# Kernel tuning notes

Measured on AMD Instinct MI355X. Metric: run time of the kernel, lower is better.

Reference implementation:

```python
import math
import jax, jax.numpy as jnp
import numpy as np

RM = 100.0      # r_max
RN = 1000       # r_dsc
LMAX = 2
MATCH_FRAC = 0.1
PARA1 = 1.0
RD = RM / RN    # radial step
NE = 4096       # batch of trial energies


def setup_inputs() -> dict:
    key = jax.random.key(0)
    # small negative energies (bound-state regime) to keep the exponential
    # Numerov growth over 900 steps within fp32 range
    init_energy = -(jax.random.uniform(key, (NE,), dtype=jnp.float32) * 0.01 + 0.005)
    return {"init_energy": init_energy}


def _disc_solve(sol0, factor, limit):
    # sol0: (5, n_e, L) initial 5-point window; factor: (rn, n_e, L)
    # Numerov-style 4-step recurrence, vectorized coefficients + lax.scan
    c = 3.0 / 40.0 * RD ** 2
    idx = jnp.arange(1, limit - 5)
    f0 = factor[idx]
    f1 = factor[idx + 1]
    f2 = factor[idx + 2]
    f3 = factor[idx + 3]
    f4 = factor[idx + 4]
    denom = 1.0 - c * f4
    a = -1.0 + c * f0 / denom
    b = 2.0 + (13.0 / 15.0) * RD ** 2 * f1 / denom
    cc = -2.0 + (7.0 / 60.0) * RD ** 2 * f2 / denom
    d = 2.0 + (13.0 / 15.0) * RD ** 2 * f3 / denom

    def step(prev, coef):
        ca, cb, ccc, cd = coef
        new4 = ca * prev[1] + cb * prev[2] + ccc * prev[3] + cd * prev[4]
        new = jnp.concatenate([prev[1:], new4[None]], axis=0)  # shift window
        return new, new

    _, rest = jax.lax.scan(step, sol0, (a, b, cc, d))
    return jnp.concatenate([sol0[None], rest], axis=0)  # (limit-5, 5, n_e, L)


def _derivative(func, at):
    return (25.0 * func[at - 1] - 48.0 * func[at - 2] + 36.0 * func[at - 3]
            - 16.0 * func[at - 4] + 3.0 * func[at - 5]) / (12.0 * RD)


def _integrate(func):
    # faithful to original: integrand squares `func` again (func is u**2 here)
    M = func.shape[0] // 4 - 1
    g0 = func[0:4 * M:4]
    g1 = func[1:4 * M:4]
    g2 = func[2:4 * M:4]
    g3 = func[3:4 * M:4]
    g4 = func[4::4][:M]
    integrand = (7.0 * (g0 ** 2 + g4 ** 2) + 32.0 * (g1 ** 2 + g3 ** 2)
                 + 12.0 * g2) * (2.0 * RD / 45.0)
    return integrand.sum(axis=0)


def _forward(init_energy):
    L = LMAX + 1
    dt = init_energy.dtype
    n_e = init_energy.shape[0]
    r = jnp.linspace(RM / RN, RM, RN, dtype=dt).reshape(RN, 1, 1)
    l = jnp.arange(L, dtype=dt).reshape(1, 1, L)

    energy = jnp.broadcast_to(init_energy[:, None], (n_e, L))  # (n_e, L)
    e_val = energy[None]                                       # (1, n_e, L)
    # coulomb potential -1/r; factor: (rn, n_e, L)
    factor = l * (l + 1) / r ** 2 + PARA1 * (-e_val - 1.0 / r)

    # left (r->0) initial window: u ~ r^(l+1) + r^(l+2)/(2(l+1)) * (-para_1)
    r0 = jnp.linspace(RD, 5 * RD, 5, dtype=dt).reshape(5, 1, 1)
    u_zero_init = jnp.broadcast_to(
        r0 ** (l + 1) - r0 ** (l + 2) / (2.0 * (l + 1)) * PARA1, (5, n_e, L))

    # right (r->r_max) initial window: r * truncated spherical-bessel series
    r_inf = jnp.linspace(RM - 4 * RD, RM, 5, dtype=dt).reshape(5, 1, 1)
    fact = jnp.array([math.prod([2 * li + 1 for li in range(lm + 1)])
                      for lm in range(L)], dtype=dt)  # [1, 3, 15]
    x = r_inf * jnp.sqrt(jnp.abs(e_val))              # (5, n_e, L)
    base = x ** l / fact
    t1 = x ** 2 / 2.0 / (2 * l + 3)
    t2 = (x ** 2 / 2.0) ** 2 / (2.0 * (2 * l + 3) * (2 * l + 5))
    u_infty_init = jnp.broadcast_to(r_inf * (base * (1.0 + t1 + t2)), (5, n_e, L))

    match = int(RN * MATCH_FRAC)  # 100
    uz = _disc_solve(u_zero_init, factor, match)                     # (95, 5, n_e, L)
    ui = _disc_solve(u_infty_init, factor[::-1], RN - match)[::-1]   # (895, 5, n_e, L)
    u_zero = jnp.concatenate([uz[0], uz[:, 4]], axis=0)    # (100, n_e, L)
    u_infty = jnp.concatenate([ui[0], ui[:, 4]], axis=0)   # (900, n_e, L)

    lfunc_in = _derivative(u_zero, match) / u_zero[-1]
    # faithful: the trailing flip acts on the energy axis of the (n_e, L) result
    lfunc_out = _derivative(u_infty[::-1], RN - match)[::-1] / u_infty[0]
    integ_in = _integrate(u_zero ** 2)
    integ_out = _integrate(u_infty ** 2)
    delta = -(lfunc_out - lfunc_in) / (integ_in / u_zero[-1] ** 2
                                       + integ_out / u_infty[0] ** 2)
    return (energy + delta, u_zero, u_infty)


def reference(init_energy):
    return _forward(init_energy)
```

## Files before the change

kernel.cpp:

```cpp
#include <hip/hip_runtime.h>


namespace {
constexpr int kNE    = 4096;
constexpr int kNCH   = kNE * 3;
constexpr int kMatch = 100;
constexpr float kC   = 3.0f / 40.0f * 0.01f;
constexpr float kK1  = 13.0f / 15.0f * 0.01f;
constexpr float kK2  = 7.0f / 60.0f * 0.01f;
constexpr int kSeg        = 32;
constexpr int kCPB        = 16;
constexpr int kZeroBlocks = kNCH / 512;
constexpr int kInfBlocks  = kNCH / kCPB;
}

__device__ __forceinline__ float rcp_f(float x) { return __builtin_amdgcn_rcpf(x); }
__device__ __forceinline__ float rcp_nr(float x) {
    float r = __builtin_amdgcn_rcpf(x);
    return fmaf(fmaf(-x, r, 1.0f), r, r);
}

__global__ __launch_bounds__(512) void solve_kernel(const float* __restrict__ energy,
                                                    float* __restrict__ out,
                                                    float* __restrict__ ws)
{
    __shared__ float gt[899 * 3];
    __shared__ float sPT[16][kSeg - 1][kCPB];
    __shared__ float sSt[kSeg][kCPB][4];
    float* sR4 = &sPT[0][0][0];
    float* sR2 = sR4 + kSeg * kCPB;

    const int bid = (int)blockIdx.x;
    const int tid = (int)threadIdx.x;
    float* uzero = out + kNCH;
    float* uinf  = out + kNCH + (size_t)kMatch * kNCH;

    if (bid < kZeroBlocks) {
        const int t  = bid * 512 + tid;
        const int l  = t % 3;
        const int ei = t / 3;
        const float e = energy[ei], negE = -e;
        const float ll1 = (float)(l * (l + 1));
        const float rdiv = (l == 0) ? 0.5f : ((l == 1) ? 0.25f : (1.0f/6.0f));
        float p0,p1,p2,p3,p4;
        {
            float pw[5];
            #pragma unroll
            for (int k = 0; k < 5; ++k) {
                float r = 0.1f * (float)(k + 1);
                float rl1 = (l == 0) ? r : ((l == 1) ? r*r : r*r*r);
                pw[k] = rl1 - (rl1 * r) * rdiv;
                uzero[(size_t)k * kNCH + t] = pw[k];
            }
            uzero[(size_t)5 * kNCH + t] = pw[4];
            p0=pw[0]; p1=pw[1]; p2=pw[2]; p3=pw[3]; p4=pw[4];
        }
        float acc4, acc2;
        {
            float q0=p0*p0, q1=p1*p1, q2=p2*p2, q3=p3*p3, q4=p4*p4;
            acc4 = 7.0f*q0*q0 + 32.0f*q1*q1 + 32.0f*q3*q3 + 14.0f*q4*q4 + 32.0f*q4*q4;
            acc2 = q2;
        }
        float f0, f1, f2, f3;
        {
            float i1 = rcp_f(0.2f), i2 = rcp_f(0.3f), i3 = rcp_f(0.4f), i4 = rcp_f(0.5f);
            f0 = fmaf(i1, fmaf(ll1, i1, -1.0f), negE);
            f1 = fmaf(i2, fmaf(ll1, i2, -1.0f), negE);
            f2 = fmaf(i3, fmaf(ll1, i3, -1.0f), negE);
            f3 = fmaf(i4, fmaf(ll1, i4, -1.0f), negE);
        }
        float* ptr = uzero + (size_t)6 * kNCH + t;
        #pragma unroll 4
        for (int j = 5; j <= 98; ++j) {
            float ri = rcp_f(fmaf((float)j, 0.1f, 0.1f));
            float f4 = fmaf(ri, fmaf(ll1, ri, -1.0f), negE);
            float iv = rcp_f(fmaf(-kC, f4, 1.0f));
            float a  = fmaf(kC  * f0, iv, -1.0f);
            float b  = fmaf(kK1 * f1, iv,  2.0f);
            float cc = fmaf(kK2 * f2, iv, -2.0f);
            float d  = fmaf(kK1 * f3, iv,  2.0f);
            float nw = fmaf(d, p4, fmaf(cc, p3, fmaf(b, p2, a * p1)));
            *ptr = nw; ptr += kNCH;
            float v2 = nw*nw, v4 = v2*v2;
            if (j <= 94) {
                int m = (j + 1) & 3;
                if (m == 2)      acc2 += v2;
                else if (m == 0) acc4 += 14.0f * v4;
                else             acc4 += 32.0f * v4;
            } else if (j == 95) {
                acc4 += 7.0f * v4;
            }
            f0 = f1; f1 = f2; f2 = f3; f3 = f4;
            p0 = p1; p1 = p2; p2 = p3; p3 = p4; p4 = nw;
        }
        float integ = fmaf(12.0f, acc2, acc4) * (2.0f * 0.1f / 45.0f);
        float deriv = fmaf(25.0f, p4, fmaf(-48.0f, p3, fmaf(36.0f, p2,
                      fmaf(-16.0f, p1, 3.0f * p0)))) * (1.0f / 1.2f);
        ws[2 * kNCH + t] = deriv / p4;
        ws[3 * kNCH + t] = integ / (p4 * p4);
        return;
    }

    for (int j = tid; j < 899; j += 512) {
        float ri = rcp_nr(fmaf((float)j, -0.1f, 100.0f));
        gt[j * 3 + 0] = -ri;
        gt[j * 3 + 1] = ri * fmaf(2.0f, ri, -1.0f);
        gt[j * 3 + 2] = ri * fmaf(6.0f, ri, -1.0f);
    }
    __syncthreads();

    const int b = bid - kZeroBlocks;
    const int g = tid & 15;
    const int s = tid >> 4;
    const int t = b * kCPB + g;
    const int l  = t % 3;
    const int ei = t / 3;
    const float e = energy[ei], negE = -e;
    const int jstart = 5 + 28 * s;

    const float ff0 = gt[(jstart - 4) * 3 + l] + negE;
    const float ff1 = gt[(jstart - 3) * 3 + l] + negE;
    const float ff2 = gt[(jstart - 2) * 3 + l] + negE;
    const float ff3 = gt[(jstart - 1) * 3 + l] + negE;
    float F0 = ff0, F1 = ff1, F2 = ff2, F3 = ff3;
    const float* gp0 = &gt[jstart * 3 + l];
    const float* gp = gp0;

    float ca, cb, cc_, cd;
#define COEF(FA,FB,FC,FD) \
    { float f4 = *gp + negE; gp += 3; \
      float x  = kC * f4; \
      float iv = fmaf(x, x, x) + 1.0f; \
      ca  = fmaf(kC  * FA, iv, -1.0f); \
      cb  = fmaf(kK1 * FB, iv,  2.0f); \
      cc_ = fmaf(kK2 * FC, iv, -2.0f); \
      cd  = fmaf(kK1 * FD, iv,  2.0f); \
      FA = f4; }

#define MSTEP(FA,FB,FC,FD,RA,RB,RC,RD) \
    { COEF(FA,FB,FC,FD) \
      RA[0] = fmaf(cd,RD[0], fmaf(cc_,RC[0], fmaf(cb,RB[0], ca*RA[0]))); \
      RA[1] = fmaf(cd,RD[1], fmaf(cc_,RC[1], fmaf(cb,RB[1], ca*RA[1]))); \
      RA[2] = fmaf(cd,RD[2], fmaf(cc_,RC[2], fmaf(cb,RB[2], ca*RA[2]))); \
      RA[3] = fmaf(cd,RD[3], fmaf(cc_,RC[3], fmaf(cb,RB[3], ca*RA[3]))); }

    if (s < kSeg - 1) {
        float ra[4] = {1,0,0,0}, rb[4] = {0,1,0,0}, rc[4] = {0,0,1,0}, rd[4] = {0,0,0,1};
        for (int it = 0; it < 7; ++it) {
            MSTEP(F0,F1,F2,F3, ra,rb,rc,rd)
            MSTEP(F1,F2,F3,F0, rb,rc,rd,ra)
            MSTEP(F2,F3,F0,F1, rc,rd,ra,rb)
            MSTEP(F3,F0,F1,F2, rd,ra,rb,rc)
        }
        #pragma unroll
        for (int c = 0; c < 4; ++c) {
            sPT[0*4+c][s][g] = ra[c];
            sPT[1*4+c][s][g] = rb[c];
            sPT[2*4+c][s][g] = rc[c];
            sPT[3*4+c][s][g] = rd[c];
        }
    }
    __syncthreads();

    if (s == 0) {
        const float se  = sqrtf(fabsf(e));
        const float rfc = (l == 0) ? 1.0f : ((l == 1) ? (1.0f/3.0f) : (1.0f/15.0f));
        const float rt1 = (l == 0) ? (1.0f/3.0f) : ((l == 1) ? (1.0f/5.0f) : (1.0f/7.0f));
        const float rt2 = (l == 0) ? (1.0f/30.0f) : ((l == 1) ? (1.0f/70.0f) : (1.0f/126.0f));
        float pw[5];
        #pragma unroll
        for (int k = 0; k < 5; ++k) {
            float rinf = 99.6f + 0.1f * (float)k;
            float x  = rinf * se;
            float xl = (l == 0) ? 1.0f : ((l == 1) ? x : x * x);
            float h  = x * x * 0.5f;
            pw[k] = rinf * (xl * rfc * (1.0f + h * rt1 + (h * h) * rt2));
        }
        uinf[(size_t)899 * kNCH + t] = pw[4];
        float st0 = pw[1], st1 = pw[2], st2 = pw[3], st3 = pw[4];
        for (int ss = 0; ss < kSeg; ++ss) {
            sSt[ss][g][0] = st0; sSt[ss][g][1] = st1;
            sSt[ss][g][2] = st2; sSt[ss][g][3] = st3;
            if (ss < kSeg - 1) {
                float n0 = fmaf(sPT[ 3][ss][g],st3, fmaf(sPT[ 2][ss][g],st2,
                           fmaf(sPT[ 1][ss][g],st1, sPT[ 0][ss][g]*st0)));
                float n1 = fmaf(sPT[ 7][ss][g],st3, fmaf(sPT[ 6][ss][g],st2,
                           fmaf(sPT[ 5][ss][g],st1, sPT[ 4][ss][g]*st0)));
                float n2 = fmaf(sPT[11][ss][g],st3, fmaf(sPT[10][ss][g],st2,
                           fmaf(sPT[ 9][ss][g],st1, sPT[ 8][ss][g]*st0)));
                float n3 = fmaf(sPT[15][ss][g],st3, fmaf(sPT[14][ss][g],st2,
                           fmaf(sPT[13][ss][g],st1, sPT[12][ss][g]*st0)));
                st0 = n0; st1 = n1; st2 = n2; st3 = n3;
            }
        }
    }
    __syncthreads();

    gp = gp0;
    F0 = ff0; F1 = ff1; F2 = ff2; F3 = ff3;
    int j = jstart;
    float p0 = sSt[s][g][0], p1 = sSt[s][g][1], p2 = sSt[s][g][2], p3 = sSt[s][g][3];
    float acc4 = 0.0f, acc2 = 0.0f;
    float* ptr = uinf + (size_t)(903 - jstart) * kNCH + t;
#define RSTEP(FA,FB,FC,FD,PA,PB,PC,PD) \
    { COEF(FA,FB,FC,FD) \
      float nw = fmaf(cd,PD, fmaf(cc_,PC, fmaf(cb,PB, ca*PA))); \
      PA = nw; *ptr = nw; ptr -= kNCH; \
      float v2 = nw*nw, v4 = v2*v2; \
      if (j >= 8) { int m = j & 3; \
        if (m == 1) acc2 += v2; \
        else acc4 += ((m == 3) ? 14.0f : 32.0f) * v4; } \
      else if (j == 7) acc4 += 7.0f * v4; \
      ++j; }

    float h0 = 0.0f;
    if (s < kSeg - 1) {
        for (int it = 0; it < 7; ++it) {
            RSTEP(F0,F1,F2,F3, p0,p1,p2,p3)
            RSTEP(F1,F2,F3,F0, p1,p2,p3,p0)
            RSTEP(F2,F3,F0,F1, p2,p3,p0,p1)
            RSTEP(F3,F0,F1,F2, p3,p0,p1,p2)
        }
    } else {
        for (int it = 0; it < 6; ++it) {
            RSTEP(F0,F1,F2,F3, p0,p1,p2,p3)
            RSTEP(F1,F2,F3,F0, p1,p2,p3,p0)
            RSTEP(F2,F3,F0,F1, p2,p3,p0,p1)
            RSTEP(F3,F0,F1,F2, p3,p0,p1,p2)
        }
        RSTEP(F0,F1,F2,F3, p0,p1,p2,p3)
        h0 = p1;
        RSTEP(F1,F2,F3,F0, p1,p2,p3,p0)
    }
    sR4[s * kCPB + g] = acc4;
    sR2[s * kCPB + g] = acc2;
    __syncthreads();

    if (s == kSeg - 1) {
        float a4 = 0.0f, a2 = 0.0f;
        #pragma unroll
        for (int ss = 0; ss < kSeg; ++ss) {
            a4 += sR4[ss * kCPB + g]; a2 += sR2[ss * kCPB + g];
        }
        float h1 = p2, h2 = p3, h3 = p0, h4 = p1;
        uinf[(size_t)0 * kNCH + t] = h0;
        uinf[(size_t)1 * kNCH + t] = h1;
        uinf[(size_t)2 * kNCH + t] = h2;
        uinf[(size_t)3 * kNCH + t] = h3;
        uinf[(size_t)4 * kNCH + t] = h4;
        float q0 = h0*h0, q1 = h1*h1, q2 = h2*h2, q3 = h3*h3, q4 = h4*h4;
        a4 += 7.0f*q0*q0 + 32.0f*q1*q1 + 32.0f*q3*q3 + 14.0f*q4*q4;
        a2 += q2;
        float integ = fmaf(12.0f, a2, a4) * (2.0f * 0.1f / 45.0f);
        float deriv = fmaf(25.0f, h0, fmaf(-48.0f, h1, fmaf(36.0f, h2,
                      fmaf(-16.0f, h3, 3.0f * h4)))) * (1.0f / 1.2f);
        ws[t]        = deriv / h0;
        ws[kNCH + t] = integ / (h0 * h0);
    }
#undef RSTEP
#undef MSTEP
#undef COEF
}

__global__ __launch_bounds__(256) void final_kernel(const float* __restrict__ energy,
                                                    const float* __restrict__ ws,
                                                    float* __restrict__ out)
{
    int t = (int)blockIdx.x * 256 + (int)threadIdx.x;
    if (t >= kNCH) return;
    int l = t % 3, ei = t / 3;
    float lf_out = ws[(kNE - 1 - ei) * 3 + l];
    float lf_in  = ws[2 * kNCH + t];
    float den    = ws[kNCH + t] + ws[3 * kNCH + t];
    out[t] = energy[ei] - (lf_out - lf_in) / den;
}

extern "C" void kernel_launch(void* const* d_in, const int* in_sizes, int n_in,
                              void* d_out, int out_size, void* d_ws, size_t ws_size,
                              hipStream_t stream) {
    (void)in_sizes; (void)n_in; (void)out_size; (void)ws_size;
    const float* energy = (const float*)d_in[0];
    float* out = (float*)d_out;
    float* ws  = (float*)d_ws;
    solve_kernel<<<kZeroBlocks + kInfBlocks, 512, 0, stream>>>(energy, out, ws);
    final_kernel<<<kNCH / 256, 256, 0, stream>>>(energy, ws, out);
}
```

Measured before the change: 93.13 us.

## Split fused solver into separate matrix, combine, and replay kernels via global workspace

Replaces the single solve kernel, which used block-level shared memory and __syncthreads to chain the segmented parallel-scan phases, with five separate launches: zero-side solve plus table build, per-segment transfer matrices, a sequential state combine, a segment replay, and a final reduction. Intermediate matrices, segment states and partial integrals now go through global workspace instead of LDS. The thread mapping also changes from 16 channels × 32 segments per block to 256 channels per block with the segment index taken from the block index, which should give coalesced global accesses. The cost is extra launch overhead and global memory traffic of roughly 16×31×12288 floats for the matrices, and the combine phase runs on only 48 blocks.

```diff
diff --git a/kernel.cpp b/kernel.cpp
--- a/kernel.cpp
+++ b/kernel.cpp
@@ -8,10 +8,16 @@
 constexpr float kC   = 3.0f / 40.0f * 0.01f;
 constexpr float kK1  = 13.0f / 15.0f * 0.01f;
 constexpr float kK2  = 7.0f / 60.0f * 0.01f;
-constexpr int kSeg        = 32;
-constexpr int kCPB        = 16;
-constexpr int kZeroBlocks = kNCH / 512;
-constexpr int kInfBlocks  = kNCH / kCPB;
+constexpr int kSeg   = 32;
+
+constexpr size_t W_LF_IN = 0;
+constexpr size_t W_IG_IN = 12288;
+constexpr size_t W_GT    = 24576;
+constexpr size_t W_MAT   = 32768;
+constexpr size_t W_ST    = W_MAT + (size_t)16 * 31 * 12288;
+constexpr size_t W_A4    = W_ST  + (size_t)4 * 32 * 12288;
+constexpr size_t W_A2    = W_A4  + (size_t)32 * 12288;
+constexpr size_t W_HD    = W_A2  + (size_t)32 * 12288;
 }
 
 __device__ __forceinline__ float rcp_f(float x) { return __builtin_amdgcn_rcpf(x); }
@@ -20,115 +26,8 @@
     return fmaf(fmaf(-x, r, 1.0f), r, r);
 }
 
-__global__ __launch_bounds__(512) void solve_kernel(const float* __restrict__ energy,
-                                                    float* __restrict__ out,
-                                                    float* __restrict__ ws)
-{
-    __shared__ float gt[899 * 3];
-    __shared__ float sPT[16][kSeg - 1][kCPB];
-    __shared__ float sSt[kSeg][kCPB][4];
-    float* sR4 = &sPT[0][0][0];
-    float* sR2 = sR4 + kSeg * kCPB;
-
-    const int bid = (int)blockIdx.x;
-    const int tid = (int)threadIdx.x;
-    float* uzero = out + kNCH;
-    float* uinf  = out + kNCH + (size_t)kMatch * kNCH;
-
-    if (bid < kZeroBlocks) {
-        const int t  = bid * 512 + tid;
-        const int l  = t % 3;
-        const int ei = t / 3;
-        const float e = energy[ei], negE = -e;
-        const float ll1 = (float)(l * (l + 1));
-        const float rdiv = (l == 0) ? 0.5f : ((l == 1) ? 0.25f : (1.0f/6.0f));
-        float p0,p1,p2,p3,p4;
-        {
-            float pw[5];
-            #pragma unroll
-            for (int k = 0; k < 5; ++k) {
-                float r = 0.1f * (float)(k + 1);
-                float rl1 = (l == 0) ? r : ((l == 1) ? r*r : r*r*r);
-                pw[k] = rl1 - (rl1 * r) * rdiv;
-                uzero[(size_t)k * kNCH + t] = pw[k];
-            }
-            uzero[(size_t)5 * kNCH + t] = pw[4];
-            p0=pw[0]; p1=pw[1]; p2=pw[2]; p3=pw[3]; p4=pw[4];
-        }
-        float acc4, acc2;
-        {
-            float q0=p0*p0, q1=p1*p1, q2=p2*p2, q3=p3*p3, q4=p4*p4;
-            acc4 = 7.0f*q0*q0 + 32.0f*q1*q1 + 32.0f*q3*q3 + 14.0f*q4*q4 + 32.0f*q4*q4;
-            acc2 = q2;
-        }
-        float f0, f1, f2, f3;
-        {
-            float i1 = rcp_f(0.2f), i2 = rcp_f(0.3f), i3 = rcp_f(0.4f), i4 = rcp_f(0.5f);
-            f0 = fmaf(i1, fmaf(ll1, i1, -1.0f), negE);
-            f1 = fmaf(i2, fmaf(ll1, i2, -1.0f), negE);
-            f2 = fmaf(i3, fmaf(ll1, i3, -1.0f), negE);
-            f3 = fmaf(i4, fmaf(ll1, i4, -1.0f), negE);
-        }
-        float* ptr = uzero + (size_t)6 * kNCH + t;
-        #pragma unroll 4
-        for (int j = 5; j <= 98; ++j) {
-            float ri = rcp_f(fmaf((float)j, 0.1f, 0.1f));
-            float f4 = fmaf(ri, fmaf(ll1, ri, -1.0f), negE);
-            float iv = rcp_f(fmaf(-kC, f4, 1.0f));
-            float a  = fmaf(kC  * f0, iv, -1.0f);
-            float b  = fmaf(kK1 * f1, iv,  2.0f);
-            float cc = fmaf(kK2 * f2, iv, -2.0f);
-            float d  = fmaf(kK1 * f3, iv,  2.0f);
-            float nw = fmaf(d, p4, fmaf(cc, p3, fmaf(b, p2, a * p1)));
-            *ptr = nw; ptr += kNCH;
-            float v2 = nw*nw, v4 = v2*v2;
-            if (j <= 94) {
-                int m = (j + 1) & 3;
-                if (m == 2)      acc2 += v2;
-                else if (m == 0) acc4 += 14.0f * v4;
-                else             acc4 += 32.0f * v4;
-            } else if (j == 95) {
-                acc4 += 7.0f * v4;
-            }
-            f0 = f1; f1 = f2; f2 = f3; f3 = f4;
-            p0 = p1; p1 = p2; p2 = p3; p3 = p4; p4 = nw;
-        }
-        float integ = fmaf(12.0f, acc2, acc4) * (2.0f * 0.1f / 45.0f);
-        float deriv = fmaf(25.0f, p4, fmaf(-48.0f, p3, fmaf(36.0f, p2,
-                      fmaf(-16.0f, p1, 3.0f * p0)))) * (1.0f / 1.2f);
-        ws[2 * kNCH + t] = deriv / p4;
-        ws[3 * kNCH + t] = integ / (p4 * p4);
-        return;
-    }
-
-    for (int j = tid; j < 899; j += 512) {
-        float ri = rcp_nr(fmaf((float)j, -0.1f, 100.0f));
-        gt[j * 3 + 0] = -ri;
-        gt[j * 3 + 1] = ri * fmaf(2.0f, ri, -1.0f);
-        gt[j * 3 + 2] = ri * fmaf(6.0f, ri, -1.0f);
-    }
-    __syncthreads();
-
-    const int b = bid - kZeroBlocks;
-    const int g = tid & 15;
-    const int s = tid >> 4;
-    const int t = b * kCPB + g;
-    const int l  = t % 3;
-    const int ei = t / 3;
-    const float e = energy[ei], negE = -e;
-    const int jstart = 5 + 28 * s;
-
-    const float ff0 = gt[(jstart - 4) * 3 + l] + negE;
-    const float ff1 = gt[(jstart - 3) * 3 + l] + negE;
-    const float ff2 = gt[(jstart - 2) * 3 + l] + negE;
-    const float ff3 = gt[(jstart - 1) * 3 + l] + negE;
-    float F0 = ff0, F1 = ff1, F2 = ff2, F3 = ff3;
-    const float* gp0 = &gt[jstart * 3 + l];
-    const float* gp = gp0;
-
-    float ca, cb, cc_, cd;
-#define COEF(FA,FB,FC,FD) \
-    { float f4 = *gp + negE; gp += 3; \
+#define COEF(GQ,FA,FB,FC,FD) \
+    { float f4 = *GQ + negE; GQ += 3; \
       float x  = kC * f4; \
       float iv = fmaf(x, x, x) + 1.0f; \
       ca  = fmaf(kC  * FA, iv, -1.0f); \
@@ -137,73 +36,193 @@
       cd  = fmaf(kK1 * FD, iv,  2.0f); \
       FA = f4; }
 
+__global__ __launch_bounds__(256) void k_zero(const float* __restrict__ energy,
+                                              float* __restrict__ out,
+                                              float* __restrict__ ws)
+{
+    const int t = (int)blockIdx.x * 256 + (int)threadIdx.x;
+
+    if (t < 899) {
+        float ri = rcp_nr(fmaf((float)t, -0.1f, 100.0f));
+        ws[W_GT + t * 3 + 0] = -ri;
+        ws[W_GT + t * 3 + 1] = ri * fmaf(2.0f, ri, -1.0f);
+        ws[W_GT + t * 3 + 2] = ri * fmaf(6.0f, ri, -1.0f);
+    }
+
+    const int l  = t % 3;
+    const int ei = t / 3;
+    const float e = energy[ei], negE = -e;
+    const float ll1 = (float)(l * (l + 1));
+    const float rdiv = (l == 0) ? 0.5f : ((l == 1) ? 0.25f : (1.0f/6.0f));
+    float* uzero = out + kNCH;
+    float p0,p1,p2,p3,p4;
+    {
+        float pw[5];
+        #pragma unroll
+        for (int k = 0; k < 5; ++k) {
+            float r = 0.1f * (float)(k + 1);
+            float rl1 = (l == 0) ? r : ((l == 1) ? r*r : r*r*r);
+            pw[k] = rl1 - (rl1 * r) * rdiv;
+            uzero[(size_t)k * kNCH + t] = pw[k];
+        }
+        uzero[(size_t)5 * kNCH + t] = pw[4];
+        p0=pw[0]; p1=pw[1]; p2=pw[2]; p3=pw[3]; p4=pw[4];
+    }
+    float acc4, acc2;
+    {
+        float q0=p0*p0, q1=p1*p1, q2=p2*p2, q3=p3*p3, q4=p4*p4;
+        acc4 = 7.0f*q0*q0 + 32.0f*q1*q1 + 32.0f*q3*q3 + 14.0f*q4*q4 + 32.0f*q4*q4;
+        acc2 = q2;
+    }
+    float f0, f1, f2, f3;
+    {
+        float i1 = rcp_f(0.2f), i2 = rcp_f(0.3f), i3 = rcp_f(0.4f), i4 = rcp_f(0.5f);
+        f0 = fmaf(i1, fmaf(ll1, i1, -1.0f), negE);
+        f1 = fmaf(i2, fmaf(ll1, i2, -1.0f), negE);
+        f2 = fmaf(i3, fmaf(ll1, i3, -1.0f), negE);
+        f3 = fmaf(i4, fmaf(ll1, i4, -1.0f), negE);
+    }
+    float* ptr = uzero + (size_t)6 * kNCH + t;
+    #pragma unroll 4
+    for (int j = 5; j <= 98; ++j) {
+        float ri = rcp_f(fmaf((float)j, 0.1f, 0.1f));
+        float f4 = fmaf(ri, fmaf(ll1, ri, -1.0f), negE);
+        float iv = rcp_f(fmaf(-kC, f4, 1.0f));
+        float a  = fmaf(kC  * f0, iv, -1.0f);
+        float b  = fmaf(kK1 * f1, iv,  2.0f);
+        float cc = fmaf(kK2 * f2, iv, -2.0f);
+        float d  = fmaf(kK1 * f3, iv,  2.0f);
+        float nw = fmaf(d, p4, fmaf(cc, p3, fmaf(b, p2, a * p1)));
+        *ptr = nw; ptr += kNCH;
+        float v2 = nw*nw, v4 = v2*v2;
+        if (j <= 94) {
+            int m = (j + 1) & 3;
+            if (m == 2)      acc2 += v2;
+            else if (m == 0) acc4 += 14.0f * v4;
+            else             acc4 += 32.0f * v4;
+        } else if (j == 95) {
+            acc4 += 7.0f * v4;
+        }
+        f0 = f1; f1 = f2; f2 = f3; f3 = f4;
+        p0 = p1; p1 = p2; p2 = p3; p3 = p4; p4 = nw;
+    }
+    float integ = fmaf(12.0f, acc2, acc4) * (2.0f * 0.1f / 45.0f);
+    float deriv = fmaf(25.0f, p4, fmaf(-48.0f, p3, fmaf(36.0f, p2,
+                  fmaf(-16.0f, p1, 3.0f * p0)))) * (1.0f / 1.2f);
+    ws[W_LF_IN + t] = deriv / p4;
+    ws[W_IG_IN + t] = integ / (p4 * p4);
+}
+
+__global__ __launch_bounds__(256) void k_mat(const float* __restrict__ energy,
+                                             float* __restrict__ ws)
+{
+    const int bid = (int)blockIdx.x;
+    const int s = bid / 48;
+    const int t = (bid % 48) * 256 + (int)threadIdx.x;
+    const int l = t % 3, ei = t / 3;
+    const float negE = -energy[ei];
+    const int jstart = 5 + 28 * s;
+    const float* gq = ws + W_GT + (size_t)jstart * 3 + l;
+    float F0 = gq[-12] + negE, F1 = gq[-9] + negE, F2 = gq[-6] + negE, F3 = gq[-3] + negE;
+
+    float ca, cb, cc_, cd;
+    float ra[4] = {1,0,0,0}, rb[4] = {0,1,0,0}, rc[4] = {0,0,1,0}, rd[4] = {0,0,0,1};
 #define MSTEP(FA,FB,FC,FD,RA,RB,RC,RD) \
-    { COEF(FA,FB,FC,FD) \
+    { COEF(gq,FA,FB,FC,FD) \
       RA[0] = fmaf(cd,RD[0], fmaf(cc_,RC[0], fmaf(cb,RB[0], ca*RA[0]))); \
       RA[1] = fmaf(cd,RD[1], fmaf(cc_,RC[1], fmaf(cb,RB[1], ca*RA[1]))); \
       RA[2] = fmaf(cd,RD[2], fmaf(cc_,RC[2], fmaf(cb,RB[2], ca*RA[2]))); \
       RA[3] = fmaf(cd,RD[3], fmaf(cc_,RC[3], fmaf(cb,RB[3], ca*RA[3]))); }
-
-    if (s < kSeg - 1) {
-        float ra[4] = {1,0,0,0}, rb[4] = {0,1,0,0}, rc[4] = {0,0,1,0}, rd[4] = {0,0,0,1};
-        for (int it = 0; it < 7; ++it) {
-            MSTEP(F0,F1,F2,F3, ra,rb,rc,rd)
-            MSTEP(F1,F2,F3,F0, rb,rc,rd,ra)
-            MSTEP(F2,F3,F0,F1, rc,rd,ra,rb)
-            MSTEP(F3,F0,F1,F2, rd,ra,rb,rc)
-        }
-        #pragma unroll
-        for (int c = 0; c < 4; ++c) {
-            sPT[0*4+c][s][g] = ra[c];
-            sPT[1*4+c][s][g] = rb[c];
-            sPT[2*4+c][s][g] = rc[c];
-            sPT[3*4+c][s][g] = rd[c];
-        }
-    }
-    __syncthreads();
-
-    if (s == 0) {
-        const float se  = sqrtf(fabsf(e));
-        const float rfc = (l == 0) ? 1.0f : ((l == 1) ? (1.0f/3.0f) : (1.0f/15.0f));
-        const float rt1 = (l == 0) ? (1.0f/3.0f) : ((l == 1) ? (1.0f/5.0f) : (1.0f/7.0f));
-        const float rt2 = (l == 0) ? (1.0f/30.0f) : ((l == 1) ? (1.0f/70.0f) : (1.0f/126.0f));
-        float pw[5];
-        #pragma unroll
-        for (int k = 0; k < 5; ++k) {
-            float rinf = 99.6f + 0.1f * (float)k;
-            float x  = rinf * se;
-            float xl = (l == 0) ? 1.0f : ((l == 1) ? x : x * x);
-            float h  = x * x * 0.5f;
-            pw[k] = rinf * (xl * rfc * (1.0f + h * rt1 + (h * h) * rt2));
-        }
-        uinf[(size_t)899 * kNCH + t] = pw[4];
-        float st0 = pw[1], st1 = pw[2], st2 = pw[3], st3 = pw[4];
-        for (int ss = 0; ss < kSeg; ++ss) {
-            sSt[ss][g][0] = st0; sSt[ss][g][1] = st1;
-            sSt[ss][g][2] = st2; sSt[ss][g][3] = st3;
-            if (ss < kSeg - 1) {
-                float n0 = fmaf(sPT[ 3][ss][g],st3, fmaf(sPT[ 2][ss][g],st2,
-                           fmaf(sPT[ 1][ss][g],st1, sPT[ 0][ss][g]*st0)));
-                float n1 = fmaf(sPT[ 7][ss][g],st3, fmaf(sPT[ 6][ss][g],st2,
-                           fmaf(sPT[ 5][ss][g],st1, sPT[ 4][ss][g]*st0)));
-                float n2 = fmaf(sPT[11][ss][g],st3, fmaf(sPT[10][ss][g],st2,
-                           fmaf(sPT[ 9][ss][g],st1, sPT[ 8][ss][g]*st0)));
-                float n3 = fmaf(sPT[15][ss][g],st3, fmaf(sPT[14][ss][g],st2,
-                           fmaf(sPT[13][ss][g],st1, sPT[12][ss][g]*st0)));
-                st0 = n0; st1 = n1; st2 = n2; st3 = n3;
-            }
-        }
-    }
-    __syncthreads();
-
-    gp = gp0;
-    F0 = ff0; F1 = ff1; F2 = ff2; F3 = ff3;
+    #pragma unroll
+    for (int it = 0; it < 7; ++it) {
+        MSTEP(F0,F1,F2,F3, ra,rb,rc,rd)
+        MSTEP(F1,F2,F3,F0, rb,rc,rd,ra)
+        MSTEP(F2,F3,F0,F1, rc,rd,ra,rb)
+        MSTEP(F3,F0,F1,F2, rd,ra,rb,rc)
+    }
+#undef MSTEP
+    float* m = ws + W_MAT + t;
+    #pragma unroll
+    for (int c = 0; c < 4; ++c) {
+        m[(size_t)(( 0 + c) * 31 + s) * kNCH] = ra[c];
+        m[(size_t)(( 4 + c) * 31 + s) * kNCH] = rb[c];
+        m[(size_t)(( 8 + c) * 31 + s) * kNCH] = rc[c];
+        m[(size_t)((12 + c) * 31 + s) * kNCH] = rd[c];
+    }
+}
+
+__global__ __launch_bounds__(256) void k_comb(const float* __restrict__ energy,
+                                              float* __restrict__ out,
+                                              float* __restrict__ ws)
+{
+    const int t = (int)blockIdx.x * 256 + (int)threadIdx.x;
+    const int l = t % 3, ei = t / 3;
+    const float e = energy[ei];
+    float* uinf = out + kNCH + (size_t)kMatch * kNCH;
+
+    const float se  = sqrtf(fabsf(e));
+    const float rfc = (l == 0) ? 1.0f : ((l == 1) ? (1.0f/3.0f) : (1.0f/15.0f));
+    const float rt1 = (l == 0) ? (1.0f/3.0f) : ((l == 1) ? (1.0f/5.0f) : (1.0f/7.0f));
+    const float rt2 = (l == 0) ? (1.0f/30.0f) : ((l == 1) ? (1.0f/70.0f) : (1.0f/126.0f));
+    float pw[5];
+    #pragma unroll
+    for (int k = 0; k < 5; ++k) {
+        float rinf = 99.6f + 0.1f * (float)k;
+        float x  = rinf * se;
+        float xl = (l == 0) ? 1.0f : ((l == 1) ? x : x * x);
+        float h  = x * x * 0.5f;
+        pw[k] = rinf * (xl * rfc * (1.0f + h * rt1 + (h * h) * rt2));
+    }
+    uinf[(size_t)899 * kNCH + t] = pw[4];
+
+    float st0 = pw[1], st1 = pw[2], st2 = pw[3], st3 = pw[4];
+    const float* m  = ws + W_MAT + t;
+    float* stp      = ws + W_ST + t;
+    #pragma unroll
+    for (int ss = 0; ss < kSeg; ++ss) {
+        stp[(size_t)(ss*4 + 0) * kNCH] = st0;
+        stp[(size_t)(ss*4 + 1) * kNCH] = st1;
+        stp[(size_t)(ss*4 + 2) * kNCH] = st2;
+        stp[(size_t)(ss*4 + 3) * kNCH] = st3;
+        if (ss < kSeg - 1) {
+            float M[16];
+            #pragma unroll
+            for (int i = 0; i < 16; ++i) M[i] = m[(size_t)(i * 31 + ss) * kNCH];
+            float n0 = fmaf(M[ 3],st3, fmaf(M[ 2],st2, fmaf(M[ 1],st1, M[ 0]*st0)));
+            float n1 = fmaf(M[ 7],st3, fmaf(M[ 6],st2, fmaf(M[ 5],st1, M[ 4]*st0)));
+            float n2 = fmaf(M[11],st3, fmaf(M[10],st2, fmaf(M[ 9],st1, M[ 8]*st0)));
+            float n3 = fmaf(M[15],st3, fmaf(M[14],st2, fmaf(M[13],st1, M[12]*st0)));
+            st0 = n0; st1 = n1; st2 = n2; st3 = n3;
+        }
+    }
+}
+
+__global__ __launch_bounds__(256) void k_replay(const float* __restrict__ energy,
+                                                float* __restrict__ out,
+                                                float* __restrict__ ws)
+{
+    const int bid = (int)blockIdx.x;
+    const int s = bid / 48;
+    const int t = (bid % 48) * 256 + (int)threadIdx.x;
+    const int l = t % 3, ei = t / 3;
+    const float negE = -energy[ei];
+    float* uinf = out + kNCH + (size_t)kMatch * kNCH;
+    const int jstart = 5 + 28 * s;
     int j = jstart;
-    float p0 = sSt[s][g][0], p1 = sSt[s][g][1], p2 = sSt[s][g][2], p3 = sSt[s][g][3];
+
+    const float* gq = ws + W_GT + (size_t)jstart * 3 + l;
+    float F0 = gq[-12] + negE, F1 = gq[-9] + negE, F2 = gq[-6] + negE, F3 = gq[-3] + negE;
+    const float* stp = ws + W_ST + t;
+    float p0 = stp[(size_t)(s*4 + 0) * kNCH];
+    float p1 = stp[(size_t)(s*4 + 1) * kNCH];
+    float p2 = stp[(size_t)(s*4 + 2) * kNCH];
+    float p3 = stp[(size_t)(s*4 + 3) * kNCH];
+
+    float ca, cb, cc_, cd;
     float acc4 = 0.0f, acc2 = 0.0f;
     float* ptr = uinf + (size_t)(903 - jstart) * kNCH + t;
 #define RSTEP(FA,FB,FC,FD,PA,PB,PC,PD) \
-    { COEF(FA,FB,FC,FD) \
+    { COEF(gq,FA,FB,FC,FD) \
       float nw = fmaf(cd,PD, fmaf(cc_,PC, fmaf(cb,PB, ca*PA))); \
       PA = nw; *ptr = nw; ptr -= kNCH; \
       float v2 = nw*nw, v4 = v2*v2; \
@@ -215,6 +234,7 @@
 
     float h0 = 0.0f;
     if (s < kSeg - 1) {
+        #pragma unroll
         for (int it = 0; it < 7; ++it) {
             RSTEP(F0,F1,F2,F3, p0,p1,p2,p3)
             RSTEP(F1,F2,F3,F0, p1,p2,p3,p0)
@@ -222,6 +242,7 @@
             RSTEP(F3,F0,F1,F2, p3,p0,p1,p2)
         }
     } else {
+        #pragma unroll
         for (int it = 0; it < 6; ++it) {
             RSTEP(F0,F1,F2,F3, p0,p1,p2,p3)
             RSTEP(F1,F2,F3,F0, p1,p2,p3,p0)
@@ -232,46 +253,57 @@
         h0 = p1;
         RSTEP(F1,F2,F3,F0, p1,p2,p3,p0)
     }
-    sR4[s * kCPB + g] = acc4;
-    sR2[s * kCPB + g] = acc2;
-    __syncthreads();
-
+#undef RSTEP
+    ws[W_A4 + (size_t)s * kNCH + t] = acc4;
+    ws[W_A2 + (size_t)s * kNCH + t] = acc2;
     if (s == kSeg - 1) {
-        float a4 = 0.0f, a2 = 0.0f;
-        #pragma unroll
-        for (int ss = 0; ss < kSeg; ++ss) {
-            a4 += sR4[ss * kCPB + g]; a2 += sR2[ss * kCPB + g];
-        }
         float h1 = p2, h2 = p3, h3 = p0, h4 = p1;
         uinf[(size_t)0 * kNCH + t] = h0;
         uinf[(size_t)1 * kNCH + t] = h1;
         uinf[(size_t)2 * kNCH + t] = h2;
         uinf[(size_t)3 * kNCH + t] = h3;
         uinf[(size_t)4 * kNCH + t] = h4;
-        float q0 = h0*h0, q1 = h1*h1, q2 = h2*h2, q3 = h3*h3, q4 = h4*h4;
-        a4 += 7.0f*q0*q0 + 32.0f*q1*q1 + 32.0f*q3*q3 + 14.0f*q4*q4;
-        a2 += q2;
-        float integ = fmaf(12.0f, a2, a4) * (2.0f * 0.1f / 45.0f);
-        float deriv = fmaf(25.0f, h0, fmaf(-48.0f, h1, fmaf(36.0f, h2,
-                      fmaf(-16.0f, h3, 3.0f * h4)))) * (1.0f / 1.2f);
-        ws[t]        = deriv / h0;
-        ws[kNCH + t] = integ / (h0 * h0);
-    }
-#undef RSTEP
-#undef MSTEP
-#undef COEF
+        ws[W_HD + (size_t)0 * kNCH + t] = h0;
+        ws[W_HD + (size_t)1 * kNCH + t] = h1;
+        ws[W_HD + (size_t)2 * kNCH + t] = h2;
+        ws[W_HD + (size_t)3 * kNCH + t] = h3;
+        ws[W_HD + (size_t)4 * kNCH + t] = h4;
+    }
 }
 
 __global__ __launch_bounds__(256) void final_kernel(const float* __restrict__ energy,
                                                     const float* __restrict__ ws,
                                                     float* __restrict__ out)
 {
-    int t = (int)blockIdx.x * 256 + (int)threadIdx.x;
-    if (t >= kNCH) return;
-    int l = t % 3, ei = t / 3;
-    float lf_out = ws[(kNE - 1 - ei) * 3 + l];
-    float lf_in  = ws[2 * kNCH + t];
-    float den    = ws[kNCH + t] + ws[3 * kNCH + t];
+    const int t = (int)blockIdx.x * 256 + (int)threadIdx.x;
+    const int l = t % 3, ei = t / 3;
+    float a4 = 0.0f, a2 = 0.0f;
+    #pragma unroll
+    for (int ss = 0; ss < kSeg; ++ss) {
+        a4 += ws[W_A4 + (size_t)ss * kNCH + t];
+        a2 += ws[W_A2 + (size_t)ss * kNCH + t];
+    }
+    float h0 = ws[W_HD + (size_t)0 * kNCH + t];
+    float h1 = ws[W_HD + (size_t)1 * kNCH + t];
+    float h2 = ws[W_HD + (size_t)2 * kNCH + t];
+    float h3 = ws[W_HD + (size_t)3 * kNCH + t];
+    float h4 = ws[W_HD + (size_t)4 * kNCH + t];
+    float q0 = h0*h0, q1 = h1*h1, q2 = h2*h2, q3 = h3*h3, q4 = h4*h4;
+    a4 += 7.0f*q0*q0 + 32.0f*q1*q1 + 32.0f*q3*q3 + 14.0f*q4*q4;
+    a2 += q2;
+    float integ = fmaf(12.0f, a2, a4) * (2.0f * 0.1f / 45.0f);
+
+    const int tp = (kNE - 1 - ei) * 3 + l;
+    float g0 = ws[W_HD + (size_t)0 * kNCH + tp];
+    float g1 = ws[W_HD + (size_t)1 * kNCH + tp];
+    float g2 = ws[W_HD + (size_t)2 * kNCH + tp];
+    float g3 = ws[W_HD + (size_t)3 * kNCH + tp];
+    float g4 = ws[W_HD + (size_t)4 * kNCH + tp];
+    float lf_out = (fmaf(25.0f, g0, fmaf(-48.0f, g1, fmaf(36.0f, g2,
+                   fmaf(-16.0f, g3, 3.0f * g4)))) * (1.0f / 1.2f)) / g0;
+
+    float den = integ / (h0 * h0) + ws[W_IG_IN + t];
+    float lf_in = ws[W_LF_IN + t];
     out[t] = energy[ei] - (lf_out - lf_in) / den;
 }
 
@@ -282,6 +314,9 @@
     const float* energy = (const float*)d_in[0];
     float* out = (float*)d_out;
     float* ws  = (float*)d_ws;
-    solve_kernel<<<kZeroBlocks + kInfBlocks, 512, 0, stream>>>(energy, out, ws);
-    final_kernel<<<kNCH / 256, 256, 0, stream>>>(energy, ws, out);
-}
+    k_zero  <<<48,        256, 0, stream>>>(energy, out, ws);
+    k_mat   <<<31 * 48,   256, 0, stream>>>(energy, ws);
+    k_comb  <<<48,        256, 0, stream>>>(energy, out, ws);
+    k_replay<<<32 * 48,   256, 0, stream>>>(energy, out, ws);
+    final_kernel<<<48,    256, 0, stream>>>(energy, ws, out);
+}
```

Measured after the change: 118.8 us. +27.6%, slower.

## Rebalance infinity solve to 16 segments of 32 channels with branchless accumulation

Applied to the files above, without the earlier changes.

Changes the segmented parallel scan for the outward Numerov solve from 32 segments of 16 channels to 16 segments of 32 channels, giving each segment 56 steps. The last segment overlaps the previous one so all threads run a uniform 56-step replay. The integration weighting uses per-thread weight tables with fmaf instead of branches on step index, and shared state is transposed to channel-contiguous layout. This halves the serial carry-propagation chain and doubles channels per block, but lengthens each thread's serial matrix-product and replay phases.

```diff
diff --git a/kernel.cpp b/kernel.cpp
--- a/kernel.cpp
+++ b/kernel.cpp
@@ -8,8 +8,8 @@
 constexpr float kC   = 3.0f / 40.0f * 0.01f;
 constexpr float kK1  = 13.0f / 15.0f * 0.01f;
 constexpr float kK2  = 7.0f / 60.0f * 0.01f;
-constexpr int kSeg        = 32;
-constexpr int kCPB        = 16;
+constexpr int kSeg        = 16;
+constexpr int kCPB        = 32;
 constexpr int kZeroBlocks = kNCH / 512;
 constexpr int kInfBlocks  = kNCH / kCPB;
 }
@@ -25,8 +25,8 @@
                                                     float* __restrict__ ws)
 {
     __shared__ float gt[899 * 3];
-    __shared__ float sPT[16][kSeg - 1][kCPB];
-    __shared__ float sSt[kSeg][kCPB][4];
+    __shared__ float sPT[16][15][kCPB];
+    __shared__ float sSt[kSeg][4][kCPB];
     float* sR4 = &sPT[0][0][0];
     float* sR2 = sR4 + kSeg * kCPB;
 
@@ -101,22 +101,22 @@
         return;
     }
 
-    for (int j = tid; j < 899; j += 512) {
-        float ri = rcp_nr(fmaf((float)j, -0.1f, 100.0f));
-        gt[j * 3 + 0] = -ri;
-        gt[j * 3 + 1] = ri * fmaf(2.0f, ri, -1.0f);
-        gt[j * 3 + 2] = ri * fmaf(6.0f, ri, -1.0f);
+    for (int jj = tid; jj < 899; jj += 512) {
+        float ri = rcp_nr(fmaf((float)jj, -0.1f, 100.0f));
+        gt[jj * 3 + 0] = -ri;
+        gt[jj * 3 + 1] = ri * fmaf(2.0f, ri, -1.0f);
+        gt[jj * 3 + 2] = ri * fmaf(6.0f, ri, -1.0f);
     }
     __syncthreads();
 
     const int b = bid - kZeroBlocks;
-    const int g = tid & 15;
-    const int s = tid >> 4;
+    const int g = tid & 31;
+    const int s = tid >> 5;
     const int t = b * kCPB + g;
     const int l  = t % 3;
     const int ei = t / 3;
     const float e = energy[ei], negE = -e;
-    const int jstart = 5 + 28 * s;
+    const int jstart = (s < 15) ? (5 + 56 * s) : 843;
 
     const float ff0 = gt[(jstart - 4) * 3 + l] + negE;
     const float ff1 = gt[(jstart - 3) * 3 + l] + negE;
@@ -144,9 +144,9 @@
       RA[2] = fmaf(cd,RD[2], fmaf(cc_,RC[2], fmaf(cb,RB[2], ca*RA[2]))); \
       RA[3] = fmaf(cd,RD[3], fmaf(cc_,RC[3], fmaf(cb,RB[3], ca*RA[3]))); }
 
-    if (s < kSeg - 1) {
+    if (s < 14) {
         float ra[4] = {1,0,0,0}, rb[4] = {0,1,0,0}, rc[4] = {0,0,1,0}, rd[4] = {0,0,0,1};
-        for (int it = 0; it < 7; ++it) {
+        for (int it = 0; it < 14; ++it) {
             MSTEP(F0,F1,F2,F3, ra,rb,rc,rd)
             MSTEP(F1,F2,F3,F0, rb,rc,rd,ra)
             MSTEP(F2,F3,F0,F1, rc,rd,ra,rb)
@@ -154,10 +154,23 @@
         }
         #pragma unroll
         for (int c = 0; c < 4; ++c) {
-            sPT[0*4+c][s][g] = ra[c];
-            sPT[1*4+c][s][g] = rb[c];
-            sPT[2*4+c][s][g] = rc[c];
-            sPT[3*4+c][s][g] = rd[c];
+            sPT[ 0+c][s][g] = ra[c]; sPT[ 4+c][s][g] = rb[c];
+            sPT[ 8+c][s][g] = rc[c]; sPT[12+c][s][g] = rd[c];
+        }
+    } else if (s == 14) {
+        float ra[4] = {1,0,0,0}, rb[4] = {0,1,0,0}, rc[4] = {0,0,1,0}, rd[4] = {0,0,0,1};
+        for (int it = 0; it < 13; ++it) {
+            MSTEP(F0,F1,F2,F3, ra,rb,rc,rd)
+            MSTEP(F1,F2,F3,F0, rb,rc,rd,ra)
+            MSTEP(F2,F3,F0,F1, rc,rd,ra,rb)
+            MSTEP(F3,F0,F1,F2, rd,ra,rb,rc)
+        }
+        MSTEP(F0,F1,F2,F3, ra,rb,rc,rd)
+        MSTEP(F1,F2,F3,F0, rb,rc,rd,ra)
+        #pragma unroll
+        for (int c = 0; c < 4; ++c) {
+            sPT[ 0+c][s][g] = rc[c]; sPT[ 4+c][s][g] = rd[c];
+            sPT[ 8+c][s][g] = ra[c]; sPT[12+c][s][g] = rb[c];
         }
     }
     __syncthreads();
@@ -179,8 +192,8 @@
         uinf[(size_t)899 * kNCH + t] = pw[4];
         float st0 = pw[1], st1 = pw[2], st2 = pw[3], st3 = pw[4];
         for (int ss = 0; ss < kSeg; ++ss) {
-            sSt[ss][g][0] = st0; sSt[ss][g][1] = st1;
-            sSt[ss][g][2] = st2; sSt[ss][g][3] = st3;
+            sSt[ss][0][g] = st0; sSt[ss][1][g] = st1;
+            sSt[ss][2][g] = st2; sSt[ss][3][g] = st3;
             if (ss < kSeg - 1) {
                 float n0 = fmaf(sPT[ 3][ss][g],st3, fmaf(sPT[ 2][ss][g],st2,
                            fmaf(sPT[ 1][ss][g],st1, sPT[ 0][ss][g]*st0)));
@@ -196,42 +209,42 @@
     }
     __syncthreads();
 
+    float W0[4] = {0.0f, 32.0f, 14.0f, 32.0f};
+    float V0[4] = {1.0f, 0.0f, 0.0f, 0.0f};
+    float WR[4] = {0.0f, 32.0f, 14.0f, 32.0f};
+    float VR[4] = {1.0f, 0.0f, 0.0f, 0.0f};
+    if (s == 0) {
+        W0[0]=0; V0[0]=0; W0[1]=0; V0[1]=0; W0[2]=7.0f; V0[2]=0; W0[3]=32.0f; V0[3]=0;
+    } else if (s == 15) {
+        WR[0]=14.0f; VR[0]=0; WR[1]=32.0f; VR[1]=0; WR[2]=0; VR[2]=1.0f; WR[3]=32.0f; VR[3]=0;
+        W0[0]=0; V0[0]=0; W0[1]=0; V0[1]=0; W0[2]=0; V0[2]=1.0f; W0[3]=32.0f; V0[3]=0;
+    }
+
     gp = gp0;
     F0 = ff0; F1 = ff1; F2 = ff2; F3 = ff3;
-    int j = jstart;
-    float p0 = sSt[s][g][0], p1 = sSt[s][g][1], p2 = sSt[s][g][2], p3 = sSt[s][g][3];
+    float p0 = sSt[s][0][g], p1 = sSt[s][1][g], p2 = sSt[s][2][g], p3 = sSt[s][3][g];
     float acc4 = 0.0f, acc2 = 0.0f;
     float* ptr = uinf + (size_t)(903 - jstart) * kNCH + t;
-#define RSTEP(FA,FB,FC,FD,PA,PB,PC,PD) \
+#define RSTEPW(FA,FB,FC,FD,PA,PB,PC,PD,W,V,K) \
     { COEF(FA,FB,FC,FD) \
       float nw = fmaf(cd,PD, fmaf(cc_,PC, fmaf(cb,PB, ca*PA))); \
       PA = nw; *ptr = nw; ptr -= kNCH; \
       float v2 = nw*nw, v4 = v2*v2; \
-      if (j >= 8) { int m = j & 3; \
-        if (m == 1) acc2 += v2; \
-        else acc4 += ((m == 3) ? 14.0f : 32.0f) * v4; } \
-      else if (j == 7) acc4 += 7.0f * v4; \
-      ++j; }
-
-    float h0 = 0.0f;
-    if (s < kSeg - 1) {
-        for (int it = 0; it < 7; ++it) {
-            RSTEP(F0,F1,F2,F3, p0,p1,p2,p3)
-            RSTEP(F1,F2,F3,F0, p1,p2,p3,p0)
-            RSTEP(F2,F3,F0,F1, p2,p3,p0,p1)
-            RSTEP(F3,F0,F1,F2, p3,p0,p1,p2)
-        }
-    } else {
-        for (int it = 0; it < 6; ++it) {
-            RSTEP(F0,F1,F2,F3, p0,p1,p2,p3)
-            RSTEP(F1,F2,F3,F0, p1,p2,p3,p0)
-            RSTEP(F2,F3,F0,F1, p2,p3,p0,p1)
-            RSTEP(F3,F0,F1,F2, p3,p0,p1,p2)
-        }
-        RSTEP(F0,F1,F2,F3, p0,p1,p2,p3)
-        h0 = p1;
-        RSTEP(F1,F2,F3,F0, p1,p2,p3,p0)
-    }
+      acc4 = fmaf(W[K], v4, acc4); \
+      acc2 = fmaf(V[K], v2, acc2); }
+#define GROUP(W,V) \
+    RSTEPW(F0,F1,F2,F3, p0,p1,p2,p3, W,V,0) \
+    RSTEPW(F1,F2,F3,F0, p1,p2,p3,p0, W,V,1) \
+    RSTEPW(F2,F3,F0,F1, p2,p3,p0,p1, W,V,2) \
+    RSTEPW(F3,F0,F1,F2, p3,p0,p1,p2, W,V,3)
+
+    GROUP(W0,V0)
+    for (int it = 0; it < 12; ++it) { GROUP(WR,VR) }
+    float h0 = p3;
+    GROUP(WR,VR)
+#undef GROUP
+#undef RSTEPW
+
     sR4[s * kCPB + g] = acc4;
     sR2[s * kCPB + g] = acc2;
     __syncthreads();
@@ -242,7 +255,7 @@
         for (int ss = 0; ss < kSeg; ++ss) {
             a4 += sR4[ss * kCPB + g]; a2 += sR2[ss * kCPB + g];
         }
-        float h1 = p2, h2 = p3, h3 = p0, h4 = p1;
+        float h1 = p0, h2 = p1, h3 = p2, h4 = p3;
         uinf[(size_t)0 * kNCH + t] = h0;
         uinf[(size_t)1 * kNCH + t] = h1;
         uinf[(size_t)2 * kNCH + t] = h2;
@@ -257,7 +270,6 @@
         ws[t]        = deriv / h0;
         ws[kNCH + t] = integ / (h0 * h0);
     }
-#undef RSTEP
 #undef MSTEP
 #undef COEF
 }
```

After: 87.87 us. 1.06x faster.
